# Kernel tuning notes

Measured on AMD Instinct MI355X. Metric: run time of the kernel, lower is better.

## Reference

```python
import jax, jax.numpy as jnp
import numpy as np
import math

EMBED_DIM = 128
NUM_HEADS = 16
HEAD_DIM = EMBED_DIM // NUM_HEADS  # = 8 = n_wires of the quantum circuit


def setup_inputs() -> dict:
    key = jax.random.key(0)
    k1, k2, k3 = jax.random.split(key, 3)
    B, S = 4, 2048
    x = jax.random.normal(k1, (B, S, EMBED_DIM), dtype=jnp.float32)
    # shared trainable RX angles of the single q_layer (applied to every head)
    theta = jax.random.normal(k2, (HEAD_DIM,), dtype=jnp.float32)
    w_out = jax.random.normal(k3, (EMBED_DIM, EMBED_DIM), dtype=jnp.float32) / math.sqrt(EMBED_DIM)
    mask = jnp.ones((B, S), dtype=jnp.int32)
    return {"x": x, "theta": theta, "w_out": w_out, "mask": mask}


def quantum_linear(x_head, theta):
    # Circuit: RX(x_i) encode + RX(theta_i) on wire i, CNOT chain (i, i+1),
    # then <Z_j>. For product state |psi_i> = RX(phi_i)|0>, <Z_i> = cos(phi_i),
    # and the CNOT chain gives final <Z_j> = prod_{i<=j} cos(phi_i).
    phi = x_head + theta  # [..., D] broadcast over leading dims
    return jnp.cumprod(jnp.cos(phi), axis=-1)


def reference(x, theta, w_out, mask):
    B, S, E = x.shape
    H, D = NUM_HEADS, HEAD_DIM
    xs = x.reshape(B, S, H, D)
    q = quantum_linear(xs, theta).transpose(0, 2, 1, 3)  # [B, H, S, D]; k = v = q
    scores = jnp.einsum("bhsd,bhtd->bhst", q, q) / math.sqrt(D)
    scores = jnp.where(mask[:, None, None, :] == 0, -1e9, scores)
    probs = jax.nn.softmax(scores, axis=-1)  # dropout is identity in eval
    attn = jnp.einsum("bhst,bhtd->bhsd", probs, q)
    attn = attn.transpose(0, 2, 1, 3).reshape(B, S, E)
    return attn @ w_out.T
```

## Files before the change

kernel.cpp:

```cpp
#include <hip/hip_runtime.h>
#include <hip/hip_bf16.h>
#include <hip/hip_fp16.h>

#define NB 4
#define NS 2048
#define NE 128
#define NH 16
#define ND 8

#define THALF 1024
#define NCH 32
#define VSTRIDE 1032
#define VGSTR 2056

typedef __attribute__((ext_vector_type(8))) _Float16 half8;
typedef __attribute__((ext_vector_type(4))) _Float16 half4;
typedef __attribute__((ext_vector_type(4))) float f32x4;

__device__ __forceinline__ unsigned int pkrtz(float a, float b) {
    typedef __fp16 fp16v2 __attribute__((ext_vector_type(2)));
    union { fp16v2 h; unsigned int u; } v;
    v.h = __builtin_amdgcn_cvt_pkrtz(a, b);
    return v.u;
}
__device__ __forceinline__ unsigned short f2h(float a) {
    return __half_as_ushort(__float2half(a));
}
__device__ __forceinline__ half8 mk_half8(unsigned u0, unsigned u1,
                                          unsigned u2, unsigned u3) {
    union { half8 h; unsigned u[4]; } v;
    v.u[0] = u0; v.u[1] = u1; v.u[2] = u2; v.u[3] = u3;
    return v.h;
}

__device__ __forceinline__ void qrow(const float* __restrict__ xp,
                                     const float* th, float* p) {
    float4 a = *(const float4*)xp, c = *(const float4*)(xp + 4);
    float t = 1.f;
    t *= cosf(a.x + th[0]); p[0] = t;
    t *= cosf(a.y + th[1]); p[1] = t;
    t *= cosf(a.z + th[2]); p[2] = t;
    t *= cosf(a.w + th[3]); p[3] = t;
    t *= cosf(c.x + th[4]); p[4] = t;
    t *= cosf(c.y + th[5]); p[5] = t;
    t *= cosf(c.z + th[6]); p[6] = t;
    t *= cosf(c.w + th[7]); p[7] = t;
}

__global__ __launch_bounds__(256) void qgen_kernel(
        const float* __restrict__ x,
        const float* __restrict__ theta,
        const int* __restrict__ mask,
        unsigned short* __restrict__ qg,
        unsigned short* __restrict__ vtg) {
    const int gid = blockIdx.x * 256 + threadIdx.x;
    const int b = gid >> 14;
    const int h = gid & (NH - 1);
    const int j = (gid >> 4) & 1023;
    const int s0 = 2 * j;
    const float SC = 0.71421629f;

    float th[ND];
#pragma unroll
    for (int d = 0; d < ND; d++) th[d] = theta[d];

    float p0[ND], p1[ND];
    qrow(x + ((size_t)(b * NS + s0) * NE + h * ND), th, p0);
    qrow(x + ((size_t)(b * NS + s0 + 1) * NE + h * ND), th, p1);
    const float mz0 = mask[b * NS + s0] ? 1.f : 0.f;
    const float mz1 = mask[b * NS + s0 + 1] ? 1.f : 0.f;
    const int bh = b * NH + h;

    uint4 qa, qb;
    qa.x = pkrtz(p0[0] * SC, p0[1] * SC);
    qa.y = pkrtz(p0[2] * SC, p0[3] * SC);
    qa.z = pkrtz(p0[4] * SC, p0[5] * SC);
    qa.w = pkrtz(p0[6] * SC, p0[7] * SC);
    qb.x = pkrtz(p1[0] * SC, p1[1] * SC);
    qb.y = pkrtz(p1[2] * SC, p1[3] * SC);
    qb.z = pkrtz(p1[4] * SC, p1[5] * SC);
    qb.w = pkrtz(p1[6] * SC, p1[7] * SC);
    *(uint4*)&qg[((size_t)bh * NS + s0) * ND] = qa;
    *(uint4*)&qg[((size_t)bh * NS + s0 + 1) * ND] = qb;

    const int H = s0 >> 10, r0 = s0 & 1023;
    const int chs = r0 >> 5, u = (r0 & 31) >> 1;
    const int i = (u & 1) | (((u >> 3) & 1) << 1) | (((u >> 1) & 3) << 2);
    const int col = H * THALF + chs * 32 + 2 * i;
    unsigned short* vb = vtg + (size_t)bh * 9 * VGSTR + col;
#pragma unroll
    for (int d = 0; d < ND; d++)
        *(unsigned int*)&vb[d * VGSTR] = pkrtz(p0[d] * mz0, p1[d] * mz1);
    *(unsigned int*)&vb[8 * VGSTR] = pkrtz(mz0, mz1);
}

__global__ __launch_bounds__(512) void attn_kernel(
        const unsigned short* __restrict__ qg,
        const unsigned short* __restrict__ vtg,
        unsigned short* __restrict__ mid) {
    __shared__ unsigned short qhl[THALF * ND + 24];
    __shared__ unsigned short vT[9 * VSTRIDE];

    const int bid = blockIdx.x;
    const int bh = bid >> 4;
    const int b = bh >> 4, h = bh & (NH - 1);
    const int msix = bid & 15;
    const int tid = threadIdx.x;

    const int wave = tid >> 6, lane = tid & 63;
    const int quad = lane >> 4, l15 = lane & 15;
    const int mbase = msix * 128 + wave * 16;

    if (tid < 24) qhl[THALF * ND + tid] = 0;

    half4 hz4 = {0, 0, 0, 0};
    const unsigned short* qmrow = qg + ((size_t)bh * NS + mbase + l15) * ND
                                + (quad < 2 ? quad * 4 : 0);
    half4 bm0 = (quad < 2) ? *(const half4*)qmrow : hz4;

    const int vrow = (l15 < 9) ? l15 : 8;
    const unsigned short* vbase = &vT[vrow * VSTRIDE];

    f32x4 O0 = {0.f, 0.f, 0.f, 0.f};
    const f32x4 zc = {0.f, 0.f, 0.f, 0.f};

    for (int p = 0; p < 2; p++) {
        {
            const uint4* qs = (const uint4*)(qg + ((size_t)bh * NS + p * THALF) * ND);
            uint4* qd = (uint4*)qhl;
            qd[tid] = qs[tid];
            qd[tid + 512] = qs[tid + 512];
        }
        {
            const unsigned short* vs = vtg + (size_t)bh * 9 * VGSTR + p * THALF;
            for (int jj = tid; jj < 1152; jj += 512) {
                int d = jj >> 7, c = (jj & 127) << 3;
                *(uint4*)&vT[d * VSTRIDE + c] = *(const uint4*)&vs[d * VGSTR + c];
            }
        }
        __syncthreads();

        for (int ch = 0; ch < NCH; ch++) {
            int tb = ch * 32;
            half4 at0 = *(const half4*)&qhl[(tb + l15) * ND + quad * 4];
            half4 at1 = *(const half4*)&qhl[(tb + 16 + l15) * ND + quad * 4];
            half8 vf  = *(const half8*)&vbase[tb + quad * 8];

            f32x4 s00 = __builtin_amdgcn_mfma_f32_16x16x16f16(at0, bm0, zc, 0, 0, 0);
            f32x4 s10 = __builtin_amdgcn_mfma_f32_16x16x16f16(at1, bm0, zc, 0, 0, 0);

            half8 pA0 = mk_half8(
                pkrtz(__builtin_amdgcn_exp2f(s00[0]), __builtin_amdgcn_exp2f(s00[1])),
                pkrtz(__builtin_amdgcn_exp2f(s00[2]), __builtin_amdgcn_exp2f(s00[3])),
                pkrtz(__builtin_amdgcn_exp2f(s10[0]), __builtin_amdgcn_exp2f(s10[1])),
                pkrtz(__builtin_amdgcn_exp2f(s10[2]), __builtin_amdgcn_exp2f(s10[3])));

            O0 = __builtin_amdgcn_mfma_f32_16x16x32_f16(pA0, vf, O0, 0, 0, 0);
        }
        __syncthreads();
    }

#pragma unroll
    for (int r = 0; r < 4; r++) {
        float lsum = __shfl(O0[r], (lane & 48) | 8, 64);
        float v = O0[r] / lsum;
        if (l15 < ND) {
            int m = mbase + quad * 4 + r;
            mid[(size_t)(b * NS + m) * NE + h * ND + l15] = f2h(v);
        }
    }
}

__global__ __launch_bounds__(256) void proj_kernel(
        const unsigned short* __restrict__ mid,
        const float* __restrict__ w,
        float* __restrict__ out) {
    __shared__ unsigned short wf[NE * 136];
    __shared__ unsigned short am[32 * 136];
    const int rb = blockIdx.x * 32;
    const int tid = threadIdx.x;

    for (int i = tid; i < 2048; i += 256) {
        const float* wp = w + i * 8;
        float4 a = *(const float4*)wp, c = *(const float4*)(wp + 4);
        uint4 pk;
        pk.x = pkrtz(a.x, a.y); pk.y = pkrtz(a.z, a.w);
        pk.z = pkrtz(c.x, c.y); pk.w = pkrtz(c.z, c.w);
        int n = i >> 4, k8 = (i & 15) * 8;
        *(uint4*)&wf[n * 136 + k8] = pk;
    }
    for (int i = tid; i < 512; i += 256) {
        int r = i >> 4, k8 = (i & 15) * 8;
        uint4 v = *(const uint4*)&mid[(size_t)(rb + r) * NE + k8];
        *(uint4*)&am[r * 136 + k8] = v;
    }
    __syncthreads();

    const int wave = tid >> 6, lane = tid & 63;
    const int quad = lane >> 4, l15 = lane & 15;
    const int mt = wave & 1, nh = wave >> 1;

    half8 af[4];
#pragma unroll
    for (int kt = 0; kt < 4; kt++)
        af[kt] = *(const half8*)&am[(mt * 16 + l15) * 136 + kt * 32 + quad * 8];

#pragma unroll
    for (int nt = 0; nt < 4; nt++) {
        int n0 = (nh * 4 + nt) * 16;
        f32x4 acc = {0.f, 0.f, 0.f, 0.f};
#pragma unroll
        for (int kt = 0; kt < 4; kt++) {
            half8 bf = *(const half8*)&wf[(n0 + l15) * 136 + kt * 32 + quad * 8];
            acc = __builtin_amdgcn_mfma_f32_16x16x32_f16(af[kt], bf, acc, 0, 0, 0);
        }
#pragma unroll
        for (int r = 0; r < 4; r++)
            out[(size_t)(rb + mt * 16 + quad * 4 + r) * NE + n0 + l15] = acc[r];
    }
}

extern "C" void kernel_launch(void* const* d_in, const int* in_sizes, int n_in,
                              void* d_out, int out_size, void* d_ws, size_t ws_size,
                              hipStream_t stream) {
    const float* x     = (const float*)d_in[0];
    const float* theta = (const float*)d_in[1];
    const float* w_out = (const float*)d_in[2];
    const int*   mask  = (const int*)d_in[3];
    float* out = (float*)d_out;

    unsigned short* mid16 = (unsigned short*)d_ws;
    unsigned short* qg  = mid16 + (size_t)NB * NS * NE;
    unsigned short* vtg = qg + (size_t)NB * NH * NS * ND;

    qgen_kernel<<<NB * NH * NS / 2 / 256, 256, 0, stream>>>(x, theta, mask, qg, vtg);
    attn_kernel<<<NB * NH * 16, 512, 0, stream>>>(qg, vtg, mid16);
    proj_kernel<<<NB * NS / 32, 256, 0, stream>>>(mid16, w_out, out);
}
```

Baseline: 103.7 us.

## Convert w_out to fp16 once in qgen and drop LDS staging in proj kernel

The fp32-to-fp16 conversion of w_out moves out of every proj block and into block 0 of qgen, which writes a single fp16 copy to workspace. proj_kernel now uses 16-row tiles with 8 waves, each owning 16 output columns, and loads MFMA operands straight from global memory with no shared-memory staging or barrier. The qgen thread mapping also changes so that consecutive threads walk sequence positions within one head rather than heads within one position. The intent is to remove the redundant per-block conversion of the weight matrix and the LDS round trip. In exchange, block 0 of qgen does extra serial work, and the direct global loads are strided and rely on cache hits.

```diff
diff --git a/kernel.cpp b/kernel.cpp
--- a/kernel.cpp
+++ b/kernel.cpp
@@ -51,14 +51,27 @@
         const float* __restrict__ x,
         const float* __restrict__ theta,
         const int* __restrict__ mask,
+        const float* __restrict__ w,
         unsigned short* __restrict__ qg,
-        unsigned short* __restrict__ vtg) {
+        unsigned short* __restrict__ vtg,
+        unsigned short* __restrict__ wf16) {
     const int gid = blockIdx.x * 256 + threadIdx.x;
-    const int b = gid >> 14;
-    const int h = gid & (NH - 1);
-    const int j = (gid >> 4) & 1023;
+    const int bh = gid >> 10;
+    const int b = bh >> 4, h = bh & (NH - 1);
+    const int j = gid & 1023;
     const int s0 = 2 * j;
     const float SC = 0.71421629f;
+
+    if (blockIdx.x == 0) {
+        for (int i = threadIdx.x; i < 2048; i += 256) {
+            const float* wp = w + i * 8;
+            float4 a = *(const float4*)wp, c = *(const float4*)(wp + 4);
+            uint4 pk;
+            pk.x = pkrtz(a.x, a.y); pk.y = pkrtz(a.z, a.w);
+            pk.z = pkrtz(c.x, c.y); pk.w = pkrtz(c.z, c.w);
+            *(uint4*)&wf16[i * 8] = pk;
+        }
+    }
 
     float th[ND];
 #pragma unroll
@@ -69,7 +82,6 @@
     qrow(x + ((size_t)(b * NS + s0 + 1) * NE + h * ND), th, p1);
     const float mz0 = mask[b * NS + s0] ? 1.f : 0.f;
     const float mz1 = mask[b * NS + s0 + 1] ? 1.f : 0.f;
-    const int bh = b * NH + h;
 
     uint4 qa, qb;
     qa.x = pkrtz(p0[0] * SC, p0[1] * SC);
@@ -171,53 +183,26 @@
     }
 }
 
-__global__ __launch_bounds__(256) void proj_kernel(
+__global__ __launch_bounds__(512) void proj_kernel(
         const unsigned short* __restrict__ mid,
-        const float* __restrict__ w,
+        const unsigned short* __restrict__ wf16,
         float* __restrict__ out) {
-    __shared__ unsigned short wf[NE * 136];
-    __shared__ unsigned short am[32 * 136];
-    const int rb = blockIdx.x * 32;
+    const int rb = blockIdx.x * 16;
     const int tid = threadIdx.x;
-
-    for (int i = tid; i < 2048; i += 256) {
-        const float* wp = w + i * 8;
-        float4 a = *(const float4*)wp, c = *(const float4*)(wp + 4);
-        uint4 pk;
-        pk.x = pkrtz(a.x, a.y); pk.y = pkrtz(a.z, a.w);
-        pk.z = pkrtz(c.x, c.y); pk.w = pkrtz(c.z, c.w);
-        int n = i >> 4, k8 = (i & 15) * 8;
-        *(uint4*)&wf[n * 136 + k8] = pk;
-    }
-    for (int i = tid; i < 512; i += 256) {
-        int r = i >> 4, k8 = (i & 15) * 8;
-        uint4 v = *(const uint4*)&mid[(size_t)(rb + r) * NE + k8];
-        *(uint4*)&am[r * 136 + k8] = v;
-    }
-    __syncthreads();
-
-    const int wave = tid >> 6, lane = tid & 63;
+    const int wavei = tid >> 6, lane = tid & 63;
     const int quad = lane >> 4, l15 = lane & 15;
-    const int mt = wave & 1, nh = wave >> 1;
-
-    half8 af[4];
-#pragma unroll
-    for (int kt = 0; kt < 4; kt++)
-        af[kt] = *(const half8*)&am[(mt * 16 + l15) * 136 + kt * 32 + quad * 8];
-
-#pragma unroll
-    for (int nt = 0; nt < 4; nt++) {
-        int n0 = (nh * 4 + nt) * 16;
-        f32x4 acc = {0.f, 0.f, 0.f, 0.f};
-#pragma unroll
-        for (int kt = 0; kt < 4; kt++) {
-            half8 bf = *(const half8*)&wf[(n0 + l15) * 136 + kt * 32 + quad * 8];
-            acc = __builtin_amdgcn_mfma_f32_16x16x32_f16(af[kt], bf, acc, 0, 0, 0);
-        }
-#pragma unroll
-        for (int r = 0; r < 4; r++)
-            out[(size_t)(rb + mt * 16 + quad * 4 + r) * NE + n0 + l15] = acc[r];
-    }
+    const int n0 = wavei * 16;
+
+    f32x4 acc = {0.f, 0.f, 0.f, 0.f};
+#pragma unroll
+    for (int kt = 0; kt < 4; kt++) {
+        half8 af = *(const half8*)&mid[(size_t)(rb + l15) * NE + kt * 32 + quad * 8];
+        half8 bf = *(const half8*)&wf16[(n0 + l15) * NE + kt * 32 + quad * 8];
+        acc = __builtin_amdgcn_mfma_f32_16x16x32_f16(af, bf, acc, 0, 0, 0);
+    }
+#pragma unroll
+    for (int r = 0; r < 4; r++)
+        out[(size_t)(rb + quad * 4 + r) * NE + n0 + l15] = acc[r];
 }
 
 extern "C" void kernel_launch(void* const* d_in, const int* in_sizes, int n_in,
@@ -230,10 +215,12 @@
     float* out = (float*)d_out;
 
     unsigned short* mid16 = (unsigned short*)d_ws;
-    unsigned short* qg  = mid16 + (size_t)NB * NS * NE;
-    unsigned short* vtg = qg + (size_t)NB * NH * NS * ND;
-
-    qgen_kernel<<<NB * NH * NS / 2 / 256, 256, 0, stream>>>(x, theta, mask, qg, vtg);
+    unsigned short* qg   = mid16 + (size_t)NB * NS * NE;
+    unsigned short* vtg  = qg + (size_t)NB * NH * NS * ND;
+    unsigned short* wf16 = vtg + (size_t)NB * NH * 9 * VGSTR;
+
+    qgen_kernel<<<NB * NH * NS / 2 / 256, 256, 0, stream>>>(x, theta, mask, w_out,
+                                                            qg, vtg, wf16);
     attn_kernel<<<NB * NH * 16, 512, 0, stream>>>(qg, vtg, mid16);
-    proj_kernel<<<NB * NS / 32, 256, 0, stream>>>(mid16, w_out, out);
-}
+    proj_kernel<<<NB * NS / 16, 512, 0, stream>>>(mid16, wf16, out);
+}
```

After: 103.9 us. No clear change (+0.2%).
